# Performance work log

Measured on AMD Instinct MI355X. Metric: run time of the kernel, lower is better.

## Reference

```python
import jax, jax.numpy as jnp
import numpy as np

N_NODES = 50000
IN_DIM = 256
LATENT = 128
HIDDEN = 2 * LATENT  # 256


def _xavier(key, fan_in, fan_out):
    # matches nn.init.xavier_uniform_ on a [out, in] weight; we store as [in, out]
    limit = float(np.sqrt(6.0 / (fan_in + fan_out)))
    return jax.random.uniform(key, (fan_in, fan_out), jnp.float32, -limit, limit)


def setup_inputs() -> dict:
    key = jax.random.key(0)
    ks = jax.random.split(key, 8)
    x = jax.random.normal(ks[0], (N_NODES, IN_DIM), jnp.float32)
    edge_index = jax.random.randint(ks[1], (2, 800000), 0, N_NODES, jnp.int64)
    W1 = _xavier(ks[2], IN_DIM, HIDDEN)
    b1 = jnp.zeros((HIDDEN,), jnp.float32)
    Wmu = _xavier(ks[3], HIDDEN, LATENT)
    bmu = jnp.zeros((LATENT,), jnp.float32)
    Wlv = _xavier(ks[4], HIDDEN, LATENT)
    blv = jnp.zeros((LATENT,), jnp.float32)
    return {"x": x, "edge_index": edge_index, "W1": W1, "b1": b1,
            "Wmu": Wmu, "bmu": bmu, "Wlv": Wlv, "blv": blv}


def _gcn_layer(x, W, b, src, dst):
    # PyG GCNConv: h = x @ W; add self loops; symmetric norm; scatter-add; + bias
    h = x @ W  # [N, out]
    ones = jnp.ones(src.shape[0], x.dtype)
    deg = jax.ops.segment_sum(ones, dst, num_segments=N_NODES) + 1.0  # +1 for self loop
    dinv = jax.lax.rsqrt(deg)  # deg >= 1 always
    norm = dinv[src] * dinv[dst]  # [E]
    agg = jax.ops.segment_sum(h[src] * norm[:, None], dst, num_segments=N_NODES)
    agg = agg + h * (dinv * dinv)[:, None]  # self-loop contribution, norm_ii = 1/deg_i
    return agg + b


def reference(x, edge_index, W1, b1, Wmu, bmu, Wlv, blv):
    src, dst = edge_index[0], edge_index[1]
    z = _gcn_layer(x, W1, b1, src, dst)
    z = jax.nn.relu(z)
    # dropout in eval mode == identity
    mu = _gcn_layer(z, Wmu, bmu, src, dst)
    logvar = _gcn_layer(z, Wlv, blv, src, dst)
    return (mu, logvar)
```

## Files before the change

kernel.cpp:

```cpp
#include <hip/hip_runtime.h>

#define N_NODES 50000
#define E_EDGES 800000
#define D 256
#define L 128
#define CAP 64

typedef __attribute__((ext_vector_type(8))) short bf16x8;
typedef __attribute__((ext_vector_type(4))) float f32x4;

__device__ __forceinline__ float bf2f(unsigned short u) {
    union { unsigned int i; float f; } v; v.i = ((unsigned int)u) << 16; return v.f;
}
__device__ __forceinline__ unsigned short f2bf(float f) {
    union { float f; unsigned int i; } v; v.f = f;
    unsigned int r = v.i + 0x7fffu + ((v.i >> 16) & 1u);
    return (unsigned short)(r >> 16);
}

__global__ __launch_bounds__(256) void zero_i(int* __restrict__ p, int n) {
    int i = blockIdx.x * 256 + threadIdx.x;
    if (i < n) p[i] = 0;
}

__global__ __launch_bounds__(256) void fill_fixed(const int* __restrict__ src,
                                                  const int* __restrict__ dst,
                                                  int* __restrict__ cursor,
                                                  int* __restrict__ bucket) {
    int e = blockIdx.x * 256 + threadIdx.x;
    if (e >= E_EDGES) return;
    int d = dst[e];
    int pos = atomicAdd(&cursor[d], 1);
    if (pos < CAP) bucket[d * CAP + pos] = src[e];
}

__global__ __launch_bounds__(256) void dinv_fin(const int* __restrict__ cursor,
                                                float* __restrict__ dinv) {
    int i = blockIdx.x * 256 + threadIdx.x;
    if (i < N_NODES) dinv[i] = rsqrtf((float)cursor[i] + 1.0f);
}

__global__ __launch_bounds__(256) void prep_w(
    const float* __restrict__ W1, const float* __restrict__ Wmu,
    const float* __restrict__ Wlv, const float* __restrict__ bmu,
    const float* __restrict__ blv,
    unsigned short* __restrict__ W1h, unsigned short* __restrict__ W1l,
    unsigned short* __restrict__ Wch, unsigned short* __restrict__ Wcl,
    float* __restrict__ bcat) {
    int b = blockIdx.x, t = threadIdx.x;
    if (b < 256) {
        int n = b, k = t;
        float w = W1[k * 256 + n];
        unsigned short h = f2bf(w);
        W1h[n * 256 + k] = h;
        W1l[n * 256 + k] = f2bf(w - bf2f(h));
    } else {
        int n = b - 256, k = t;
        float w = (n < 128) ? Wmu[k * 128 + n] : Wlv[k * 128 + (n - 128)];
        unsigned short h = f2bf(w);
        Wch[n * 256 + k] = h;
        Wcl[n * 256 + k] = f2bf(w - bf2f(h));
        if (b == 256) bcat[t] = (t < 128) ? bmu[t] : blv[t - 128];
    }
}

__global__ __launch_bounds__(256, 3) void gemm_mfma(
    const float* __restrict__ A,
    const unsigned short* __restrict__ Bth, const unsigned short* __restrict__ Btl,
    unsigned short* __restrict__ Hout,
    float* __restrict__ mu, float* __restrict__ lv,
    const float* __restrict__ bias, int M, int mode)
{
    __shared__ unsigned short Bsh[256 * 32];
    __shared__ unsigned short Bsl[256 * 32];
    const int t = threadIdx.x;
    const int lane = t & 63, wave = t >> 6;
    const int row0 = blockIdx.x * 64 + wave * 16;
    const int m_ = lane & 15, q = lane >> 4;
    int rA = row0 + m_; if (rA >= M) rA = M - 1;
    const float* Ap = A + (size_t)rA * 256;
    const int bn = t >> 2;
    const int bc = t & 3;

    f32x4 acc[16];
    const f32x4 zf = {0.f, 0.f, 0.f, 0.f};
#pragma unroll
    for (int nt = 0; nt < 16; ++nt) acc[nt] = zf;

    for (int ks = 0; ks < 8; ++ks) {
        const int k0 = ks * 32;
        bf16x8 gbh[4], gbl[4];
#pragma unroll
        for (int i = 0; i < 4; ++i) {
            int n = bn + i * 64;
            gbh[i] = *(const bf16x8*)(Bth + n * 256 + k0 + bc * 8);
            gbl[i] = *(const bf16x8*)(Btl + n * 256 + k0 + bc * 8);
        }
        float4 av0 = *(const float4*)(Ap + k0 + q * 8);
        float4 av1 = *(const float4*)(Ap + k0 + q * 8 + 4);
        __syncthreads();
#pragma unroll
        for (int i = 0; i < 4; ++i) {
            int n = bn + i * 64;
            int cc = (bc ^ ((n >> 1) & 3)) * 8;
            *(bf16x8*)&Bsh[n * 32 + cc] = gbh[i];
            *(bf16x8*)&Bsl[n * 32 + cc] = gbl[i];
        }
        float af[8] = {av0.x, av0.y, av0.z, av0.w, av1.x, av1.y, av1.z, av1.w};
        bf16x8 ah, al;
#pragma unroll
        for (int j = 0; j < 8; ++j) {
            unsigned short h = f2bf(af[j]);
            ah[j] = (short)h;
            al[j] = (short)f2bf(af[j] - bf2f(h));
        }
        __syncthreads();
#pragma unroll
        for (int nt = 0; nt < 16; ++nt) {
            int n = nt * 16 + m_;
            int cr = (q ^ ((n >> 1) & 3)) * 8;
            bf16x8 bh = *(const bf16x8*)&Bsh[n * 32 + cr];
            bf16x8 bl = *(const bf16x8*)&Bsl[n * 32 + cr];
            acc[nt] = __builtin_amdgcn_mfma_f32_16x16x32_bf16(ah, bh, acc[nt], 0, 0, 0);
            acc[nt] = __builtin_amdgcn_mfma_f32_16x16x32_bf16(ah, bl, acc[nt], 0, 0, 0);
            acc[nt] = __builtin_amdgcn_mfma_f32_16x16x32_bf16(al, bh, acc[nt], 0, 0, 0);
        }
    }
    int rbase = row0 + q * 4;
#pragma unroll
    for (int r = 0; r < 4; ++r) {
        int grow = rbase + r;
        if (grow >= M) continue;
#pragma unroll
        for (int nt = 0; nt < 16; ++nt) {
            int gcol = nt * 16 + m_;
            float v = acc[nt][r];
            if (mode == 0) {
                Hout[(size_t)grow * 256 + gcol] = f2bf(v);
            } else {
                v += bias[gcol];
                if (gcol < 128) mu[(size_t)grow * 128 + gcol] = v;
                else            lv[(size_t)grow * 128 + (gcol - 128)] = v;
            }
        }
    }
}

__global__ __launch_bounds__(256) void gather_pre(
    const unsigned short* __restrict__ Hs,
    const int* __restrict__ bucket, const int* __restrict__ cnt_,
    const float* __restrict__ dinv, const float* __restrict__ bias,
    unsigned short* __restrict__ OutZ, float* __restrict__ OutY, int mode)
{
    int node = blockIdx.x * 4 + (threadIdx.x >> 6);
    if (node >= N_NODES) return;
    const int lane = threadIdx.x & 63;
    const int col = lane * 4;
    int cnt = cnt_[node]; if (cnt > CAP) cnt = CAP;
    float dn = dinv[node];

    int   s_l = 0;
    float w_l = 0.f;
    if (lane < cnt) {
        s_l = bucket[node * CAP + lane];
        w_l = dinv[s_l] * dn;
    }

    float sl = dn * dn;
    ushort4 h = *(const ushort4*)(Hs + (size_t)node * D + col);
    float a0 = bf2f(h.x) * sl, a1 = bf2f(h.y) * sl;
    float a2 = bf2f(h.z) * sl, a3 = bf2f(h.w) * sl;

    int j = 0;
    for (; j + 3 < cnt; j += 4) {
        int s0 = __shfl(s_l, j, 64),     s1 = __shfl(s_l, j + 1, 64);
        int s2 = __shfl(s_l, j + 2, 64), s3 = __shfl(s_l, j + 3, 64);
        float w0 = __shfl(w_l, j, 64),     w1 = __shfl(w_l, j + 1, 64);
        float w2 = __shfl(w_l, j + 2, 64), w3 = __shfl(w_l, j + 3, 64);
        ushort4 u0 = *(const ushort4*)(Hs + (size_t)s0 * D + col);
        ushort4 u1 = *(const ushort4*)(Hs + (size_t)s1 * D + col);
        ushort4 u2 = *(const ushort4*)(Hs + (size_t)s2 * D + col);
        ushort4 u3 = *(const ushort4*)(Hs + (size_t)s3 * D + col);
        a0 = fmaf(bf2f(u0.x), w0, a0); a1 = fmaf(bf2f(u0.y), w0, a1);
        a2 = fmaf(bf2f(u0.z), w0, a2); a3 = fmaf(bf2f(u0.w), w0, a3);
        a0 = fmaf(bf2f(u1.x), w1, a0); a1 = fmaf(bf2f(u1.y), w1, a1);
        a2 = fmaf(bf2f(u1.z), w1, a2); a3 = fmaf(bf2f(u1.w), w1, a3);
        a0 = fmaf(bf2f(u2.x), w2, a0); a1 = fmaf(bf2f(u2.y), w2, a1);
        a2 = fmaf(bf2f(u2.z), w2, a2); a3 = fmaf(bf2f(u2.w), w2, a3);
        a0 = fmaf(bf2f(u3.x), w3, a0); a1 = fmaf(bf2f(u3.y), w3, a1);
        a2 = fmaf(bf2f(u3.z), w3, a2); a3 = fmaf(bf2f(u3.w), w3, a3);
    }
    for (; j < cnt; ++j) {
        int s0 = __shfl(s_l, j, 64);
        float w0 = __shfl(w_l, j, 64);
        ushort4 u0 = *(const ushort4*)(Hs + (size_t)s0 * D + col);
        a0 = fmaf(bf2f(u0.x), w0, a0); a1 = fmaf(bf2f(u0.y), w0, a1);
        a2 = fmaf(bf2f(u0.z), w0, a2); a3 = fmaf(bf2f(u0.w), w0, a3);
    }

    if (mode == 0) {
        float4 b = *(const float4*)(bias + col);
        a0 = fmaxf(a0 + b.x, 0.f); a1 = fmaxf(a1 + b.y, 0.f);
        a2 = fmaxf(a2 + b.z, 0.f); a3 = fmaxf(a3 + b.w, 0.f);
        ushort4 o; o.x = f2bf(a0); o.y = f2bf(a1); o.z = f2bf(a2); o.w = f2bf(a3);
        *(ushort4*)(OutZ + (size_t)node * D + col) = o;
    } else {
        float4 o; o.x = a0; o.y = a1; o.z = a2; o.w = a3;
        *(float4*)(OutY + (size_t)node * D + col) = o;
    }
}

extern "C" void kernel_launch(void* const* d_in, const int* in_sizes, int n_in,
                              void* d_out, int out_size, void* d_ws, size_t ws_size,
                              hipStream_t stream) {
    const float* x   = (const float*)d_in[0];
    const int*   ei  = (const int*)d_in[1];
    const float* W1  = (const float*)d_in[2];
    const float* b1  = (const float*)d_in[3];
    const float* Wmu = (const float*)d_in[4];
    const float* bmu = (const float*)d_in[5];
    const float* Wlv = (const float*)d_in[6];
    const float* blv = (const float*)d_in[7];
    const int* src = ei;
    const int* dst = ei + E_EDGES;

    const size_t NF = (size_t)N_NODES * D;
    unsigned short* Hb = (unsigned short*)d_ws;
    unsigned short* Z  = Hb + NF;
    float* Y = (float*)(Z + NF);
    unsigned short* W1h = (unsigned short*)(Y + NF);
    unsigned short* W1l = W1h + 65536;
    unsigned short* Wch = W1l + 65536;
    unsigned short* Wcl = Wch + 65536;
    float* bcat = (float*)(Wcl + 65536);
    float* dinv = bcat + 256;
    int* cursor = (int*)(dinv + N_NODES);
    int* bucket = cursor + N_NODES;
    float* mu = (float*)d_out;
    float* lv = mu + (size_t)N_NODES * L;

    zero_i<<<(N_NODES + 255) / 256, 256, 0, stream>>>(cursor, N_NODES);
    fill_fixed<<<(E_EDGES + 255) / 256, 256, 0, stream>>>(src, dst, cursor, bucket);
    dinv_fin<<<(N_NODES + 255) / 256, 256, 0, stream>>>(cursor, dinv);

    prep_w<<<512, 256, 0, stream>>>(W1, Wmu, Wlv, bmu, blv, W1h, W1l, Wch, Wcl, bcat);

    const int gemm_blocks = (N_NODES + 63) / 64;
    const int gat_blocks  = (N_NODES + 3) / 4;
    gemm_mfma<<<gemm_blocks, 256, 0, stream>>>(x, W1h, W1l, Hb,
                                               nullptr, nullptr, nullptr, N_NODES, 0);
    gather_pre<<<gat_blocks, 256, 0, stream>>>(Hb, bucket, cursor, dinv, b1,
                                               Z, nullptr, 0);
    gather_pre<<<gat_blocks, 256, 0, stream>>>(Z, bucket, cursor, dinv, nullptr,
                                               nullptr, Y, 1);
    gemm_mfma<<<gemm_blocks, 256, 0, stream>>>(Y, Wch, Wcl, nullptr,
                                               mu, lv, bcat, N_NODES, 1);
}
```

Before: 346.3 us.

## Partition gather by feature column slices per XCD with atomic work queues

Replaces the one-wave-per-node gather with a persistent kernel. Each XCD, identified through a hardware register, first works a 32-column slice of the feature matrix, so that slice of H stays resident in that XCD's L2. Work is handed out in 16-node chunks through per-slice atomic queue heads. Within a wave, 8 edge groups of 8 lanes each load different neighbours and are reduced with shuffles. This trades more index and weight reloads, since each node is revisited once per slice, plus atomic and barrier overhead, for better L2 locality of the random neighbour reads.

```diff
diff --git a/kernel.cpp b/kernel.cpp
--- a/kernel.cpp
+++ b/kernel.cpp
@@ -5,6 +5,9 @@
 #define D 256
 #define L 128
 #define CAP 64
+#define NC 16
+#define NCHUNK ((N_NODES + NC - 1) / NC)
+#define XCC_GETREG_ENC (20 | (7 << 11))
 
 typedef __attribute__((ext_vector_type(8))) short bf16x8;
 typedef __attribute__((ext_vector_type(4))) float f32x4;
@@ -146,67 +149,87 @@
     }
 }
 
-__global__ __launch_bounds__(256) void gather_pre(
+__global__ __launch_bounds__(256) void gather_xcd(
     const unsigned short* __restrict__ Hs,
     const int* __restrict__ bucket, const int* __restrict__ cnt_,
     const float* __restrict__ dinv, const float* __restrict__ bias,
-    unsigned short* __restrict__ OutZ, float* __restrict__ OutY, int mode)
+    unsigned short* __restrict__ OutZ, float* __restrict__ OutY,
+    int* __restrict__ qheads, int mode)
 {
-    int node = blockIdx.x * 4 + (threadIdx.x >> 6);
-    if (node >= N_NODES) return;
-    const int lane = threadIdx.x & 63;
-    const int col = lane * 4;
-    int cnt = cnt_[node]; if (cnt > CAP) cnt = CAP;
-    float dn = dinv[node];
-
-    int   s_l = 0;
-    float w_l = 0.f;
-    if (lane < cnt) {
-        s_l = bucket[node * CAP + lane];
-        w_l = dinv[s_l] * dn;
-    }
-
-    float sl = dn * dn;
-    ushort4 h = *(const ushort4*)(Hs + (size_t)node * D + col);
-    float a0 = bf2f(h.x) * sl, a1 = bf2f(h.y) * sl;
-    float a2 = bf2f(h.z) * sl, a3 = bf2f(h.w) * sl;
-
-    int j = 0;
-    for (; j + 3 < cnt; j += 4) {
-        int s0 = __shfl(s_l, j, 64),     s1 = __shfl(s_l, j + 1, 64);
-        int s2 = __shfl(s_l, j + 2, 64), s3 = __shfl(s_l, j + 3, 64);
-        float w0 = __shfl(w_l, j, 64),     w1 = __shfl(w_l, j + 1, 64);
-        float w2 = __shfl(w_l, j + 2, 64), w3 = __shfl(w_l, j + 3, 64);
-        ushort4 u0 = *(const ushort4*)(Hs + (size_t)s0 * D + col);
-        ushort4 u1 = *(const ushort4*)(Hs + (size_t)s1 * D + col);
-        ushort4 u2 = *(const ushort4*)(Hs + (size_t)s2 * D + col);
-        ushort4 u3 = *(const ushort4*)(Hs + (size_t)s3 * D + col);
-        a0 = fmaf(bf2f(u0.x), w0, a0); a1 = fmaf(bf2f(u0.y), w0, a1);
-        a2 = fmaf(bf2f(u0.z), w0, a2); a3 = fmaf(bf2f(u0.w), w0, a3);
-        a0 = fmaf(bf2f(u1.x), w1, a0); a1 = fmaf(bf2f(u1.y), w1, a1);
-        a2 = fmaf(bf2f(u1.z), w1, a2); a3 = fmaf(bf2f(u1.w), w1, a3);
-        a0 = fmaf(bf2f(u2.x), w2, a0); a1 = fmaf(bf2f(u2.y), w2, a1);
-        a2 = fmaf(bf2f(u2.z), w2, a2); a3 = fmaf(bf2f(u2.w), w2, a3);
-        a0 = fmaf(bf2f(u3.x), w3, a0); a1 = fmaf(bf2f(u3.y), w3, a1);
-        a2 = fmaf(bf2f(u3.z), w3, a2); a3 = fmaf(bf2f(u3.w), w3, a3);
-    }
-    for (; j < cnt; ++j) {
-        int s0 = __shfl(s_l, j, 64);
-        float w0 = __shfl(w_l, j, 64);
-        ushort4 u0 = *(const ushort4*)(Hs + (size_t)s0 * D + col);
-        a0 = fmaf(bf2f(u0.x), w0, a0); a1 = fmaf(bf2f(u0.y), w0, a1);
-        a2 = fmaf(bf2f(u0.z), w0, a2); a3 = fmaf(bf2f(u0.w), w0, a3);
-    }
-
-    if (mode == 0) {
-        float4 b = *(const float4*)(bias + col);
-        a0 = fmaxf(a0 + b.x, 0.f); a1 = fmaxf(a1 + b.y, 0.f);
-        a2 = fmaxf(a2 + b.z, 0.f); a3 = fmaxf(a3 + b.w, 0.f);
-        ushort4 o; o.x = f2bf(a0); o.y = f2bf(a1); o.z = f2bf(a2); o.w = f2bf(a3);
-        *(ushort4*)(OutZ + (size_t)node * D + col) = o;
-    } else {
-        float4 o; o.x = a0; o.y = a1; o.z = a2; o.w = a3;
-        *(float4*)(OutY + (size_t)node * D + col) = o;
+    __shared__ int chunk_s;
+    const int xcd = __builtin_amdgcn_s_getreg(XCC_GETREG_ENC) & 7;
+    const int t = threadIdx.x;
+    const int wave = t >> 6, lane = t & 63;
+    const int g = lane >> 3, li = lane & 7;
+
+    for (int qi = 0; qi < 8; ++qi) {
+        const int q = (xcd + qi) & 7;
+        const int c0 = q * 32;
+        while (true) {
+            if (t == 0) chunk_s = atomicAdd(&qheads[q], 1);
+            __syncthreads();
+            const int chunk = chunk_s;
+            __syncthreads();
+            if (chunk >= NCHUNK) break;
+            const int nbase = chunk * NC + wave;
+#pragma unroll
+            for (int nn = 0; nn < NC / 4; ++nn) {
+                const int node = nbase + nn * 4;
+                if (node >= N_NODES) break;
+                int cnt = cnt_[node]; if (cnt > CAP) cnt = CAP;
+                const float dn = dinv[node];
+                int s_l = 0; float w_l = 0.f;
+                if (lane < cnt) {
+                    s_l = bucket[node * CAP + lane];
+                    w_l = dinv[s_l] * dn;
+                }
+                float a0 = 0.f, a1 = 0.f, a2 = 0.f, a3 = 0.f;
+                if (g == 0) {
+                    float sl = dn * dn;
+                    ushort4 h = *(const ushort4*)(Hs + (size_t)node * D + c0 + li * 4);
+                    a0 = bf2f(h.x) * sl; a1 = bf2f(h.y) * sl;
+                    a2 = bf2f(h.z) * sl; a3 = bf2f(h.w) * sl;
+                }
+                const int full = cnt & ~7;
+                for (int j = 0; j < full; j += 8) {
+                    int e = j + g;
+                    int s = __builtin_amdgcn_ds_bpermute(e << 2, s_l);
+                    float w = __int_as_float(
+                        __builtin_amdgcn_ds_bpermute(e << 2, __float_as_int(w_l)));
+                    ushort4 u = *(const ushort4*)(Hs + (size_t)s * D + c0 + li * 4);
+                    a0 = fmaf(bf2f(u.x), w, a0); a1 = fmaf(bf2f(u.y), w, a1);
+                    a2 = fmaf(bf2f(u.z), w, a2); a3 = fmaf(bf2f(u.w), w, a3);
+                }
+                {
+                    int e = full + g;
+                    int s = __builtin_amdgcn_ds_bpermute(e << 2, s_l);
+                    float w = __int_as_float(
+                        __builtin_amdgcn_ds_bpermute(e << 2, __float_as_int(w_l)));
+                    if (e < cnt) {
+                        ushort4 u = *(const ushort4*)(Hs + (size_t)s * D + c0 + li * 4);
+                        a0 = fmaf(bf2f(u.x), w, a0); a1 = fmaf(bf2f(u.y), w, a1);
+                        a2 = fmaf(bf2f(u.z), w, a2); a3 = fmaf(bf2f(u.w), w, a3);
+                    }
+                }
+                a0 += __shfl_xor(a0, 8, 64); a0 += __shfl_xor(a0, 16, 64); a0 += __shfl_xor(a0, 32, 64);
+                a1 += __shfl_xor(a1, 8, 64); a1 += __shfl_xor(a1, 16, 64); a1 += __shfl_xor(a1, 32, 64);
+                a2 += __shfl_xor(a2, 8, 64); a2 += __shfl_xor(a2, 16, 64); a2 += __shfl_xor(a2, 32, 64);
+                a3 += __shfl_xor(a3, 8, 64); a3 += __shfl_xor(a3, 16, 64); a3 += __shfl_xor(a3, 32, 64);
+                if (g == 0) {
+                    const int c = c0 + li * 4;
+                    if (mode == 0) {
+                        float4 b = *(const float4*)(bias + c);
+                        a0 = fmaxf(a0 + b.x, 0.f); a1 = fmaxf(a1 + b.y, 0.f);
+                        a2 = fmaxf(a2 + b.z, 0.f); a3 = fmaxf(a3 + b.w, 0.f);
+                        ushort4 o; o.x = f2bf(a0); o.y = f2bf(a1); o.z = f2bf(a2); o.w = f2bf(a3);
+                        *(ushort4*)(OutZ + (size_t)node * D + c) = o;
+                    } else {
+                        float4 o; o.x = a0; o.y = a1; o.z = a2; o.w = a3;
+                        *(float4*)(OutY + (size_t)node * D + c) = o;
+                    }
+                }
+            }
+        }
     }
 }
 
@@ -235,24 +258,25 @@
     float* bcat = (float*)(Wcl + 65536);
     float* dinv = bcat + 256;
     int* cursor = (int*)(dinv + N_NODES);
-    int* bucket = cursor + N_NODES;
+    int* qh1    = cursor + N_NODES;
+    int* qh2    = qh1 + 8;
+    int* bucket = qh2 + 8;
     float* mu = (float*)d_out;
     float* lv = mu + (size_t)N_NODES * L;
 
-    zero_i<<<(N_NODES + 255) / 256, 256, 0, stream>>>(cursor, N_NODES);
+    zero_i<<<(N_NODES + 16 + 255) / 256, 256, 0, stream>>>(cursor, N_NODES + 16);
     fill_fixed<<<(E_EDGES + 255) / 256, 256, 0, stream>>>(src, dst, cursor, bucket);
     dinv_fin<<<(N_NODES + 255) / 256, 256, 0, stream>>>(cursor, dinv);
 
     prep_w<<<512, 256, 0, stream>>>(W1, Wmu, Wlv, bmu, blv, W1h, W1l, Wch, Wcl, bcat);
 
     const int gemm_blocks = (N_NODES + 63) / 64;
-    const int gat_blocks  = (N_NODES + 3) / 4;
     gemm_mfma<<<gemm_blocks, 256, 0, stream>>>(x, W1h, W1l, Hb,
                                                nullptr, nullptr, nullptr, N_NODES, 0);
-    gather_pre<<<gat_blocks, 256, 0, stream>>>(Hb, bucket, cursor, dinv, b1,
-                                               Z, nullptr, 0);
-    gather_pre<<<gat_blocks, 256, 0, stream>>>(Z, bucket, cursor, dinv, nullptr,
-                                               nullptr, Y, 1);
+    gather_xcd<<<1024, 256, 0, stream>>>(Hb, bucket, cursor, dinv, b1,
+                                         Z, nullptr, qh1, 0);
+    gather_xcd<<<1024, 256, 0, stream>>>(Z, bucket, cursor, dinv, nullptr,
+                                         nullptr, Y, qh2, 1);
     gemm_mfma<<<gemm_blocks, 256, 0, stream>>>(Y, Wch, Wcl, nullptr,
                                                mu, lv, bcat, N_NODES, 1);
 }
```

After: 1.030 ms. +197.4%, slower.
